# Optimization experiments

Hardware: AMD Instinct MI355X
Metric: run time of the kernel (lower is better)

## Reference

```python
import jax, jax.numpy as jnp
import numpy as np

K = 16

def _local_cov(points):
    # points: [B, N, 3]. FoldingNet-style local covariance feature.
    xx = jnp.sum(points * points, axis=-1)                       # [B,N]
    inner = jnp.einsum('bnd,bmd->bnm', points, points)           # [B,N,N]
    pd = -xx[:, :, None] + 2.0 * inner - xx[:, None, :]          # negative sq dist
    _, idx = jax.lax.top_k(pd, K)                                # [B,N,K] nearest first (self at 0)
    n0 = jnp.take_along_axis(points, idx[:, :, 0][:, :, None], axis=1)  # [B,N,3]
    n1 = jnp.take_along_axis(points, idx[:, :, 1][:, :, None], axis=1)  # [B,N,3]
    cov = n0[..., :, None] * n1[..., None, :]                    # [B,N,3,3] outer product
    B, N = points.shape[0], points.shape[1]
    return jnp.concatenate([points, cov.reshape(B, N, 9)], axis=-1)     # [B,N,12]

def _stage(x, w1, b1, wr, br, w2, b2):
    h = jax.nn.relu(x @ w1 + b1)
    h = jax.nn.relu(h + (h @ wr + br))   # ResidualLinearLayer then ReLU
    return h @ w2 + b2                   # [B,N,1]

def setup_inputs() -> dict:
    key = jax.random.key(0)
    ks = jax.random.split(key, 16)
    B, N, F = 8, 4096, 512
    s = 0.02
    d = {
        'latent': jax.random.normal(ks[0], (B, N, F), jnp.float32),
        'reconstructed_points': jax.random.normal(ks[1], (B, 3, N), jnp.float32),
        's1_w1': jax.random.normal(ks[2], (F + 12, F), jnp.float32) * s,
        's1_b1': jnp.zeros((F,), jnp.float32),
        's1_wr': jax.random.normal(ks[3], (F, F), jnp.float32) * s,
        's1_br': jnp.zeros((F,), jnp.float32),
        's1_w2': jax.random.normal(ks[4], (F, 1), jnp.float32) * s,
        's1_b2': jnp.zeros((1,), jnp.float32),
        's2_w1': jax.random.normal(ks[5], (F + 1, F), jnp.float32) * s,
        's2_b1': jnp.zeros((F,), jnp.float32),
        's2_wr': jax.random.normal(ks[6], (F, F), jnp.float32) * s,
        's2_br': jnp.zeros((F,), jnp.float32),
        's2_w2': jax.random.normal(ks[7], (F, 1), jnp.float32) * s,
        's2_b2': jnp.zeros((1,), jnp.float32),
        's3_w1': jax.random.normal(ks[8], (F + 1, F), jnp.float32) * s,
        's3_b1': jnp.zeros((F,), jnp.float32),
        's3_wr': jax.random.normal(ks[9], (F, F), jnp.float32) * s,
        's3_br': jnp.zeros((F,), jnp.float32),
        's3_w2': jax.random.normal(ks[10], (F, 1), jnp.float32) * s,
        's3_b2': jnp.zeros((1,), jnp.float32),
    }
    return d

def reference(latent, reconstructed_points,
              s1_w1, s1_b1, s1_wr, s1_br, s1_w2, s1_b2,
              s2_w1, s2_b1, s2_wr, s2_br, s2_w2, s2_b2,
              s3_w1, s3_b1, s3_wr, s3_br, s3_w2, s3_b2):
    pts = jnp.transpose(reconstructed_points, (0, 2, 1))   # [B,N,3]
    local = _local_cov(pts)                                 # [B,N,12]
    f1 = jnp.concatenate([latent, local], axis=-1)
    std1 = _stage(f1, s1_w1, s1_b1, s1_wr, s1_br, s1_w2, s1_b2)
    f2 = jnp.concatenate([latent, std1], axis=-1)
    std2 = std1 + _stage(f2, s2_w1, s2_b1, s2_wr, s2_br, s2_w2, s2_b2)
    f3 = jnp.concatenate([latent, std2], axis=-1)
    std3 = std2 + _stage(f3, s3_w1, s3_b1, s3_wr, s3_br, s3_w2, s3_b2)
    return std3   # [B,N,1]
```

## Files before the change

kernel.cpp:

```cpp
#include <hip/hip_runtime.h>

typedef __bf16 bf16x8 __attribute__((ext_vector_type(8)));
typedef float f32x16 __attribute__((ext_vector_type(16)));

__device__ __forceinline__ unsigned short f2bf(float f) {
  unsigned u = __float_as_uint(f);
  u += 0x7FFFu + ((u >> 16) & 1u);
  return (unsigned short)(u >> 16);
}

__device__ __forceinline__ void gload_lds16(const void* g, void* l) {
  __builtin_amdgcn_global_load_lds((const __attribute__((address_space(1))) void*)g,
                                   (__attribute__((address_space(3))) void*)l,
                                   16, 0, 0);
}

#define NPTS 4096
#define LDX 576

__global__ __launch_bounds__(256) void convw6_kernel(
    const float* w0, const float* w1, const float* w2,
    const float* r0, const float* r1, const float* r2,
    unsigned short* d0, unsigned short* d1, unsigned short* d2,
    unsigned short* e0, unsigned short* e1, unsigned short* e2) {
  int z = blockIdx.z;
  const float* src; unsigned short* dst; int Ksrc, Kpad, addI;
  switch (z) {
    case 0: src = w0; dst = d0; Ksrc = 524; Kpad = 576; addI = 0; break;
    case 1: src = w1; dst = d1; Ksrc = 513; Kpad = 576; addI = 0; break;
    case 2: src = w2; dst = d2; Ksrc = 513; Kpad = 576; addI = 0; break;
    case 3: src = r0; dst = e0; Ksrc = 512; Kpad = 512; addI = 1; break;
    case 4: src = r1; dst = e1; Ksrc = 512; Kpad = 512; addI = 1; break;
    default: src = r2; dst = e2; Ksrc = 512; Kpad = 512; addI = 1; break;
  }
  int k0 = blockIdx.x * 32;
  if (k0 >= Kpad) return;
  __shared__ float tile[32][33];
  int n0 = blockIdx.y * 32;
  int tx = threadIdx.x & 31, ty = threadIdx.x >> 5;
#pragma unroll
  for (int r = 0; r < 32; r += 8) {
    int k = k0 + ty + r, n = n0 + tx;
    tile[ty + r][tx] = (k < Ksrc) ? src[(size_t)k * 512 + n] : 0.f;
  }
  __syncthreads();
#pragma unroll
  for (int r = 0; r < 32; r += 8) {
    int n = n0 + ty + r, k = k0 + tx;
    float v = tile[tx][ty + r];
    if (addI && n == k) v += 1.0f;
    dst[(size_t)n * Kpad + k] = f2bf(v);
  }
}

__global__ __launch_bounds__(256) void conv_latent_kernel(const float* __restrict__ latent,
                                                          unsigned short* __restrict__ X) {
  size_t idx = (size_t)blockIdx.x * 256 + threadIdx.x;
  size_t m = idx >> 7;
  int c4 = (int)(idx & 127) * 4;
  float4 v = *(const float4*)(latent + m * 512 + c4);
  ushort4 o;
  o.x = f2bf(v.x); o.y = f2bf(v.y); o.z = f2bf(v.z); o.w = f2bf(v.w);
  *(ushort4*)(X + m * LDX + c4) = o;
}

__device__ __forceinline__ void merge1(float& v, int& j, int mk) {
  float ov = __shfl_xor(v, mk); int oj = __shfl_xor(j, mk);
  bool take = (ov > v) || (ov == v && oj < j);
  v = take ? ov : v; j = take ? oj : j;
}

__global__ __launch_bounds__(512) void knn_kernel(const float* __restrict__ rp,
                                                  unsigned short* __restrict__ X) {
  __shared__ float4 P[NPTS];
  int b = blockIdx.y;
  const float* base = rp + (size_t)b * 3 * NPTS;
  for (int j = threadIdx.x; j < NPTS; j += 512) {
    float x = base[j], y = base[NPTS + j], z = base[2 * NPTS + j];
    float xx = __fadd_rn(__fadd_rn(__fmul_rn(x, x), __fmul_rn(y, y)), __fmul_rn(z, z));
    P[j] = make_float4(x, y, z, -xx);
  }
  __syncthreads();
  int wave = threadIdx.x >> 6, lane = threadIdx.x & 63;
  int grp = lane >> 4, slice = lane & 15;
  int il0 = wave * 8 + grp * 2;
  int ia = blockIdx.x * 64 + il0;
  int ib = ia + 1;
  float4 pa = P[ia], pb = P[ib];
  float ax = 2.f * pa.x, ay = 2.f * pa.y, az = 2.f * pa.z;
  float bx = 2.f * pb.x, by = 2.f * pb.y, bz = 2.f * pb.z;
  float va = -3.4e38f, vb = -3.4e38f;
  int ta = 0, tb = 0;
  int sta = ((ia & 15) == slice) ? (ia >> 4) : -1;
  int stb = ((ib & 15) == slice) ? (ib >> 4) : -1;
  const float4* pp = P + slice;
#pragma unroll 8
  for (int t = 0; t < NPTS / 16; ++t) {
    float4 pj = pp[t * 16];
    float ea = __builtin_fmaf(ax, pj.x, __builtin_fmaf(ay, pj.y,
               __builtin_fmaf(az, pj.z, pj.w)));
    float eb = __builtin_fmaf(bx, pj.x, __builtin_fmaf(by, pj.y,
               __builtin_fmaf(bz, pj.z, pj.w)));
    ea = (t == sta) ? -3.4e38f : ea;
    eb = (t == stb) ? -3.4e38f : eb;
    bool ca = ea > va; va = ca ? ea : va; ta = ca ? t : ta;
    bool cb = eb > vb; vb = cb ? eb : vb; tb = cb ? t : tb;
  }
  int ja = ta * 16 + slice, jb = tb * 16 + slice;
#pragma unroll
  for (int mk = 1; mk <= 8; mk <<= 1) {
    merge1(va, ja, mk);
    merge1(vb, jb, mk);
  }
  if (slice == 0) {
#pragma unroll
    for (int p = 0; p < 2; ++p) {
      float4 pi = (p == 0) ? pa : pb;
      float4 p1 = P[(p == 0) ? ja : jb];
      size_t row = (size_t)b * NPTS + ia + p;
      unsigned short* xp = X + row * LDX + 512;
      float vals[12] = { pi.x, pi.y, pi.z,
                         pi.x * p1.x, pi.x * p1.y, pi.x * p1.z,
                         pi.y * p1.x, pi.y * p1.y, pi.y * p1.z,
                         pi.z * p1.x, pi.z * p1.y, pi.z * p1.z };
#pragma unroll
      for (int k = 0; k < 12; ++k) xp[k] = f2bf(vals[k]);
#pragma unroll
      for (int k = 12; k < 32; ++k) xp[k] = 0;
    }
  }
}

#define BM 256
#define BN 128
#define BK 64
#define GRP 520

__global__ __launch_bounds__(512) void gemm_relu_kernel(
    const unsigned short* __restrict__ Xb, const unsigned short* __restrict__ Wt,
    const float* __restrict__ bias, unsigned short* __restrict__ H,
    int K, int ldx, int ldw) {
  __shared__ unsigned short As[32 * GRP];
  __shared__ unsigned short Bs[16 * GRP];
  const int t = threadIdx.x;
  const int wave = t >> 6, lane = t & 63;
  const int m0 = blockIdx.y * BM, n0 = blockIdx.x * BN;
  const int wm = (wave >> 1) * 64, wn = (wave & 1) * 64;
  const int srow = lane >> 3;
  const int sslot = (lane & 7) ^ srow;
  const int l31 = lane & 31, hi = lane >> 5;
  const int w7 = l31 & 7, g2 = l31 >> 3;
  f32x16 acc[2][2] = {};
  for (int kt = 0; kt < K; kt += BK) {
#pragma unroll
    for (int r = 0; r < 4; ++r) {
      int ga = wave + r * 8;
      gload_lds16(Xb + (size_t)(m0 + ga * 8 + srow) * ldx + kt + sslot * 8, As + ga * GRP);
    }
#pragma unroll
    for (int r = 0; r < 2; ++r) {
      int gb = wave + r * 8;
      gload_lds16(Wt + (size_t)(n0 + gb * 8 + srow) * ldw + kt + sslot * 8, Bs + gb * GRP);
    }
    __syncthreads();
#pragma unroll
    for (int ks = 0; ks < 4; ++ks) {
      int qx = (ks * 2 + hi) ^ w7;
      bf16x8 a[2], bb[2];
#pragma unroll
      for (int i = 0; i < 2; ++i)
        a[i] = *(const bf16x8*)(As + ((wm >> 3) + i * 4 + g2) * GRP + w7 * 64 + qx * 8);
#pragma unroll
      for (int j = 0; j < 2; ++j)
        bb[j] = *(const bf16x8*)(Bs + ((wn >> 3) + j * 4 + g2) * GRP + w7 * 64 + qx * 8);
#pragma unroll
      for (int i = 0; i < 2; ++i)
#pragma unroll
        for (int j = 0; j < 2; ++j)
          acc[i][j] = __builtin_amdgcn_mfma_f32_32x32x16_bf16(a[i], bb[j], acc[i][j], 0, 0, 0);
    }
    __syncthreads();
  }
#pragma unroll
  for (int j = 0; j < 2; ++j) {
    int col = n0 + wn + j * 32 + l31;
    float bv = bias[col];
#pragma unroll
    for (int i = 0; i < 2; ++i) {
#pragma unroll
      for (int rg = 0; rg < 16; ++rg) {
        int row = m0 + wm + i * 32 + (rg & 3) + 8 * (rg >> 2) + 4 * hi;
        float v = acc[i][j][rg] + bv;
        v = v > 0.f ? v : 0.f;
        H[(size_t)row * 512 + col] = f2bf(v);
      }
    }
  }
}

__global__ __launch_bounds__(512) void gemm_res_kernel(
    const unsigned short* __restrict__ H1, const unsigned short* __restrict__ Wt,
    const float* __restrict__ br, const float* __restrict__ w2,
    float* __restrict__ so) {
  __shared__ unsigned short As[32 * GRP];
  __shared__ unsigned short Bs[16 * GRP];
  const int t = threadIdx.x;
  const int wave = t >> 6, lane = t & 63;
  const int m0 = blockIdx.y * BM, n0 = blockIdx.x * BN;
  const int wm = (wave >> 1) * 64, wn = (wave & 1) * 64;
  const int srow = lane >> 3;
  const int sslot = (lane & 7) ^ srow;
  const int l31 = lane & 31, hi = lane >> 5;
  const int w7 = l31 & 7, g2 = l31 >> 3;
  f32x16 acc[2][2] = {};
  for (int kt = 0; kt < 512; kt += BK) {
#pragma unroll
    for (int r = 0; r < 4; ++r) {
      int ga = wave + r * 8;
      gload_lds16(H1 + (size_t)(m0 + ga * 8 + srow) * 512 + kt + sslot * 8, As + ga * GRP);
    }
#pragma unroll
    for (int r = 0; r < 2; ++r) {
      int gb = wave + r * 8;
      gload_lds16(Wt + (size_t)(n0 + gb * 8 + srow) * 512 + kt + sslot * 8, Bs + gb * GRP);
    }
    __syncthreads();
#pragma unroll
    for (int ks = 0; ks < 4; ++ks) {
      int qx = (ks * 2 + hi) ^ w7;
      bf16x8 a[2], bb[2];
#pragma unroll
      for (int i = 0; i < 2; ++i)
        a[i] = *(const bf16x8*)(As + ((wm >> 3) + i * 4 + g2) * GRP + w7 * 64 + qx * 8);
#pragma unroll
      for (int j = 0; j < 2; ++j)
        bb[j] = *(const bf16x8*)(Bs + ((wn >> 3) + j * 4 + g2) * GRP + w7 * 64 + qx * 8);
#pragma unroll
      for (int i = 0; i < 2; ++i)
#pragma unroll
        for (int j = 0; j < 2; ++j)
          acc[i][j] = __builtin_amdgcn_mfma_f32_32x32x16_bf16(a[i], bb[j], acc[i][j], 0, 0, 0);
    }
    __syncthreads();
  }
  float pr[2][16];
#pragma unroll
  for (int i = 0; i < 2; ++i)
#pragma unroll
    for (int rg = 0; rg < 16; ++rg) pr[i][rg] = 0.f;
#pragma unroll
  for (int j = 0; j < 2; ++j) {
    int col = n0 + wn + j * 32 + l31;
    float bv = br[col], wv = w2[col];
#pragma unroll
    for (int i = 0; i < 2; ++i)
#pragma unroll
      for (int rg = 0; rg < 16; ++rg) {
        float v = acc[i][j][rg] + bv;
        v = v > 0.f ? v : 0.f;
        pr[i][rg] += v * wv;
      }
  }
#pragma unroll
  for (int i = 0; i < 2; ++i)
#pragma unroll
    for (int rg = 0; rg < 16; ++rg) {
      float s = pr[i][rg];
      s += __shfl_xor(s, 1); s += __shfl_xor(s, 2); s += __shfl_xor(s, 4);
      s += __shfl_xor(s, 8); s += __shfl_xor(s, 16);
      if (l31 == 0) {
        int row = m0 + wm + i * 32 + (rg & 3) + 8 * (rg >> 2) + 4 * hi;
        atomicAdd(&so[row], s);
      }
    }
}

__global__ __launch_bounds__(256) void init_so_kernel(float* so, const float* b2) {
  int m = blockIdx.x * 256 + threadIdx.x;
  so[m] = b2[0];
}
__global__ __launch_bounds__(256) void update_kernel(float* std_cum, float* so,
                                                     unsigned short* X,
                                                     const float* b2_next, int first) {
  int m = blockIdx.x * 256 + threadIdx.x;
  float s = so[m];
  if (!first) s += std_cum[m];
  std_cum[m] = s;
  unsigned short* xp = X + (size_t)m * LDX + 512;
  xp[0] = f2bf(s);
#pragma unroll
  for (int k = 1; k < 12; ++k) xp[k] = 0;
  so[m] = b2_next[0];
}
__global__ __launch_bounds__(256) void finalize_kernel(float* out, const float* std_cum,
                                                       const float* so) {
  int m = blockIdx.x * 256 + threadIdx.x;
  out[m] = std_cum[m] + so[m];
}

extern "C" void kernel_launch(void* const* d_in, const int* in_sizes, int n_in,
                              void* d_out, int out_size, void* d_ws, size_t ws_size,
                              hipStream_t stream) {
  const int B = 8, N = NPTS, M = B * N;
  const float* latent = (const float*)d_in[0];
  const float* rp = (const float*)d_in[1];
  const float* w1[3] = {(const float*)d_in[2], (const float*)d_in[8], (const float*)d_in[14]};
  const float* b1[3] = {(const float*)d_in[3], (const float*)d_in[9], (const float*)d_in[15]};
  const float* wr[3] = {(const float*)d_in[4], (const float*)d_in[10], (const float*)d_in[16]};
  const float* br[3] = {(const float*)d_in[5], (const float*)d_in[11], (const float*)d_in[17]};
  const float* w2[3] = {(const float*)d_in[6], (const float*)d_in[12], (const float*)d_in[18]};
  const float* b2[3] = {(const float*)d_in[7], (const float*)d_in[13], (const float*)d_in[19]};

  char* ws = (char*)d_ws;
  auto carve = [&](size_t bytes) {
    char* p = ws;
    ws += (bytes + 255) & ~(size_t)255;
    return p;
  };
  unsigned short* X  = (unsigned short*)carve((size_t)M * LDX * 2);
  unsigned short* H1 = (unsigned short*)carve((size_t)M * 512 * 2);
  unsigned short* W1t[3], *Wrt[3];
  for (int s = 0; s < 3; ++s) W1t[s] = (unsigned short*)carve((size_t)512 * LDX * 2);
  for (int s = 0; s < 3; ++s) Wrt[s] = (unsigned short*)carve((size_t)512 * 512 * 2);
  float* std_cum = (float*)carve((size_t)M * 4);
  float* so      = (float*)carve((size_t)M * 4);

  convw6_kernel<<<dim3(LDX / 32, 16, 6), 256, 0, stream>>>(
      w1[0], w1[1], w1[2], wr[0], wr[1], wr[2],
      W1t[0], W1t[1], W1t[2], Wrt[0], Wrt[1], Wrt[2]);
  conv_latent_kernel<<<(M * 128) / 256, 256, 0, stream>>>(latent, X);
  knn_kernel<<<dim3(N / 64, B), 512, 0, stream>>>(rp, X);
  init_so_kernel<<<M / 256, 256, 0, stream>>>(so, b2[0]);

  for (int s = 0; s < 3; ++s) {
    gemm_relu_kernel<<<dim3(BN / 128 * 4, M / BM), 512, 0, stream>>>(X, W1t[s], b1[s], H1,
                                                                     LDX, LDX, LDX);
    gemm_res_kernel<<<dim3(4, M / BM), 512, 0, stream>>>(H1, Wrt[s], br[s], w2[s], so);
    if (s < 2)
      update_kernel<<<M / 256, 256, 0, stream>>>(std_cum, so, X, b2[s + 1], s == 0 ? 1 : 0);
  }
  finalize_kernel<<<M / 256, 256, 0, stream>>>((float*)d_out, std_cum, so);
}
```

Measured before the change: 348.3 us.

## Apply std feature as rank-1 epilogue and reorder GEMM block mapping

For stages 2 and 3, the GEMM now runs only over the 512 latent columns and adds the single std feature as a rank-1 fp32 update (std times the last W1 row) in the epilogue. This skips the extra 64-wide K tile that held the feature and removes the per-stage write of the feature into X, and it also keeps the std term in fp32 instead of rounding it to bf16. Separately, block indices are remapped so consecutive blocks walk along M for a fixed N tile, which changes L2 reuse of the weight and activation tiles.

```diff
diff --git a/kernel.cpp b/kernel.cpp
--- a/kernel.cpp
+++ b/kernel.cpp
@@ -135,16 +135,20 @@
 #define BN 128
 #define BK 64
 #define GRP 520
+#define MBLK 128
 
 __global__ __launch_bounds__(512) void gemm_relu_kernel(
     const unsigned short* __restrict__ Xb, const unsigned short* __restrict__ Wt,
     const float* __restrict__ bias, unsigned short* __restrict__ H,
-    int K, int ldx, int ldw) {
+    int K, int ldx, int ldw,
+    const float* __restrict__ stdv, const float* __restrict__ w1row) {
   __shared__ unsigned short As[32 * GRP];
   __shared__ unsigned short Bs[16 * GRP];
   const int t = threadIdx.x;
   const int wave = t >> 6, lane = t & 63;
-  const int m0 = blockIdx.y * BM, n0 = blockIdx.x * BN;
+  const int flat = blockIdx.y * gridDim.x + blockIdx.x;
+  const int m0 = (flat & (MBLK - 1)) * BM;
+  const int n0 = (flat >> 7) * BN;
   const int wm = (wave >> 1) * 64, wn = (wave & 1) * 64;
   const int srow = lane >> 3;
   const int sslot = (lane & 7) ^ srow;
@@ -180,6 +184,21 @@
           acc[i][j] = __builtin_amdgcn_mfma_f32_32x32x16_bf16(a[i], bb[j], acc[i][j], 0, 0, 0);
     }
     __syncthreads();
+  }
+  if (w1row) {
+    float wv[2];
+#pragma unroll
+    for (int j = 0; j < 2; ++j) wv[j] = w1row[n0 + wn + j * 32 + l31];
+#pragma unroll
+    for (int i = 0; i < 2; ++i) {
+#pragma unroll
+      for (int rg = 0; rg < 16; ++rg) {
+        int row = m0 + wm + i * 32 + (rg & 3) + 8 * (rg >> 2) + 4 * hi;
+        float sv = stdv[row];
+        acc[i][0][rg] += sv * wv[0];
+        acc[i][1][rg] += sv * wv[1];
+      }
+    }
   }
 #pragma unroll
   for (int j = 0; j < 2; ++j) {
@@ -206,7 +225,9 @@
   __shared__ unsigned short Bs[16 * GRP];
   const int t = threadIdx.x;
   const int wave = t >> 6, lane = t & 63;
-  const int m0 = blockIdx.y * BM, n0 = blockIdx.x * BN;
+  const int flat = blockIdx.y * gridDim.x + blockIdx.x;
+  const int m0 = (flat & (MBLK - 1)) * BM;
+  const int n0 = (flat >> 7) * BN;
   const int wm = (wave >> 1) * 64, wn = (wave & 1) * 64;
   const int srow = lane >> 3;
   const int sslot = (lane & 7) ^ srow;
@@ -280,16 +301,11 @@
   so[m] = b2[0];
 }
 __global__ __launch_bounds__(256) void update_kernel(float* std_cum, float* so,
-                                                     unsigned short* X,
                                                      const float* b2_next, int first) {
   int m = blockIdx.x * 256 + threadIdx.x;
   float s = so[m];
   if (!first) s += std_cum[m];
   std_cum[m] = s;
-  unsigned short* xp = X + (size_t)m * LDX + 512;
-  xp[0] = f2bf(s);
-#pragma unroll
-  for (int k = 1; k < 12; ++k) xp[k] = 0;
   so[m] = b2_next[0];
 }
 __global__ __launch_bounds__(256) void finalize_kernel(float* out, const float* std_cum,
@@ -333,11 +349,16 @@
   init_so_kernel<<<M / 256, 256, 0, stream>>>(so, b2[0]);
 
   for (int s = 0; s < 3; ++s) {
-    gemm_relu_kernel<<<dim3(BN / 128 * 4, M / BM), 512, 0, stream>>>(X, W1t[s], b1[s], H1,
-                                                                     LDX, LDX, LDX);
+    if (s == 0) {
+      gemm_relu_kernel<<<dim3(512 / BN, M / BM), 512, 0, stream>>>(
+          X, W1t[s], b1[s], H1, LDX, LDX, LDX, nullptr, nullptr);
+    } else {
+      gemm_relu_kernel<<<dim3(512 / BN, M / BM), 512, 0, stream>>>(
+          X, W1t[s], b1[s], H1, 512, LDX, LDX, std_cum, w1[s] + (size_t)512 * 512);
+    }
     gemm_res_kernel<<<dim3(4, M / BM), 512, 0, stream>>>(H1, Wrt[s], br[s], w2[s], so);
     if (s < 2)
-      update_kernel<<<M / 256, 256, 0, stream>>>(std_cum, so, X, b2[s + 1], s == 0 ? 1 : 0);
+      update_kernel<<<M / 256, 256, 0, stream>>>(std_cum, so, b2[s + 1], s == 0 ? 1 : 0);
   }
   finalize_kernel<<<M / 256, 256, 0, stream>>>((float*)d_out, std_cum, so);
 }
```

Result: no change. 342.8 us (-1.6%).

## Fuse both stage GEMMs into one kernel keeping hidden activations in LDS

Applied to the files above, without the earlier changes.

Replaces the separate first-layer and residual GEMM kernels with a single fused kernel. Each block owns 64 rows and computes all 512 hidden columns, writes the ReLU output into swizzled LDS, and runs the residual GEMM from LDS with double-buffered A staging and prefetched weight tiles. The scalar std input of stages 2 and 3 is added as a rank-1 fp32 update using the original weight row, so K shrinks to 512 and update_kernel no longer writes into X. This removes the H1 round trip through global memory, at the cost of large dynamic LDS (about 150KB), low occupancy and a smaller 64-row tile per block.

```diff
diff --git a/kernel.cpp b/kernel.cpp
--- a/kernel.cpp
+++ b/kernel.cpp
@@ -17,6 +17,7 @@
 
 #define NPTS 4096
 #define LDX 576
+#define GRP 520
 
 __global__ __launch_bounds__(256) void convw6_kernel(
     const float* w0, const float* w1, const float* w2,
@@ -131,148 +132,179 @@
   }
 }
 
-#define BM 256
-#define BN 128
-#define BK 64
-#define GRP 520
-
-__global__ __launch_bounds__(512) void gemm_relu_kernel(
-    const unsigned short* __restrict__ Xb, const unsigned short* __restrict__ Wt,
-    const float* __restrict__ bias, unsigned short* __restrict__ H,
-    int K, int ldx, int ldw) {
-  __shared__ unsigned short As[32 * GRP];
-  __shared__ unsigned short Bs[16 * GRP];
+__global__ __launch_bounds__(512) void fused_stage_kernel(
+    const unsigned short* __restrict__ Xb, const unsigned short* __restrict__ W1t,
+    const float* __restrict__ b1v, const unsigned short* __restrict__ Wrt,
+    const float* __restrict__ brv, const float* __restrict__ w2v,
+    float* __restrict__ so, int K1,
+    const float* __restrict__ stdv, const float* __restrict__ w1row) {
+  extern __shared__ unsigned short S[];
+  unsigned short* HL = S;
+  unsigned short* BL = S + 64 * GRP;
+  unsigned short* AL = S + 128 * GRP;
   const int t = threadIdx.x;
   const int wave = t >> 6, lane = t & 63;
-  const int m0 = blockIdx.y * BM, n0 = blockIdx.x * BN;
-  const int wm = (wave >> 1) * 64, wn = (wave & 1) * 64;
+  const int m0 = blockIdx.x * 64;
   const int srow = lane >> 3;
   const int sslot = (lane & 7) ^ srow;
   const int l31 = lane & 31, hi = lane >> 5;
   const int w7 = l31 & 7, g2 = l31 >> 3;
+
+  const unsigned short* Arow  = Xb  + (size_t)(m0 + wave * 8 + srow) * LDX + sslot * 8;
+  const unsigned short* Wrow1 = W1t + (size_t)(64 * wave + srow) * LDX + sslot * 8;
+  const unsigned short* Wrow2 = Wrt + (size_t)(64 * wave + srow) * 512 + sslot * 8;
+
+  auto STAGE_A = [&](int buf, int kt) {
+    gload_lds16(Arow + (size_t)kt * 64, AL + buf * (8 * GRP) + wave * GRP);
+  };
+  auto STAGE_B1 = [&](int kt) {
+#pragma unroll
+    for (int r = 0; r < 8; ++r)
+      gload_lds16(Wrow1 + (size_t)r * 8 * LDX + (size_t)kt * 64, BL + (8 * wave + r) * GRP);
+  };
+  auto STAGE_B2 = [&](int kt) {
+#pragma unroll
+    for (int r = 0; r < 8; ++r)
+      gload_lds16(Wrow2 + (size_t)r * 8 * 512 + (size_t)kt * 64, BL + (8 * wave + r) * GRP);
+  };
+
+  STAGE_A(0, 0);
+  STAGE_B1(0);
+  asm volatile("s_waitcnt vmcnt(0)" ::: "memory");
+  __builtin_amdgcn_s_barrier();
+
   f32x16 acc[2][2] = {};
-  for (int kt = 0; kt < K; kt += BK) {
-#pragma unroll
-    for (int r = 0; r < 4; ++r) {
-      int ga = wave + r * 8;
-      gload_lds16(Xb + (size_t)(m0 + ga * 8 + srow) * ldx + kt + sslot * 8, As + ga * GRP);
-    }
-#pragma unroll
-    for (int r = 0; r < 2; ++r) {
-      int gb = wave + r * 8;
-      gload_lds16(Wt + (size_t)(n0 + gb * 8 + srow) * ldw + kt + sslot * 8, Bs + gb * GRP);
-    }
-    __syncthreads();
-#pragma unroll
-    for (int ks = 0; ks < 4; ++ks) {
-      int qx = (ks * 2 + hi) ^ w7;
-      bf16x8 a[2], bb[2];
+  const int nt1 = K1 / 64;
+  for (int t1 = 0; t1 < nt1; ++t1) {
+    const int cur = t1 & 1;
+    bf16x8 af[2][4], bf[2][4];
+#pragma unroll
+    for (int i = 0; i < 2; ++i)
+#pragma unroll
+      for (int ks = 0; ks < 4; ++ks)
+        af[i][ks] = *(const bf16x8*)(AL + cur * (8 * GRP) + (i * 4 + g2) * GRP +
+                                     w7 * 64 + (((2 * ks + hi) ^ w7) * 8));
+#pragma unroll
+    for (int j = 0; j < 2; ++j)
+#pragma unroll
+      for (int ks = 0; ks < 4; ++ks)
+        bf[j][ks] = *(const bf16x8*)(BL + (8 * wave + j * 4 + g2) * GRP +
+                                     w7 * 64 + (((2 * ks + hi) ^ w7) * 8));
+    asm volatile("s_waitcnt lgkmcnt(0)" ::: "memory");
+    __builtin_amdgcn_sched_barrier(0);
+    if (t1 + 1 < nt1) {
+      STAGE_A(cur ^ 1, t1 + 1);
+      STAGE_B1(t1 + 1);
+    } else {
+      STAGE_B2(0);
+    }
+#pragma unroll
+    for (int ks = 0; ks < 4; ++ks)
 #pragma unroll
       for (int i = 0; i < 2; ++i)
-        a[i] = *(const bf16x8*)(As + ((wm >> 3) + i * 4 + g2) * GRP + w7 * 64 + qx * 8);
+#pragma unroll
+        for (int j = 0; j < 2; ++j)
+          acc[i][j] = __builtin_amdgcn_mfma_f32_32x32x16_bf16(af[i][ks], bf[j][ks],
+                                                              acc[i][j], 0, 0, 0);
+    asm volatile("s_waitcnt vmcnt(0)" ::: "memory");
+    __builtin_amdgcn_sched_barrier(0);
+    __builtin_amdgcn_s_barrier();
+  }
+
+  if (w1row) {
+    float wv1[2];
+#pragma unroll
+    for (int j = 0; j < 2; ++j) wv1[j] = w1row[64 * wave + j * 32 + l31];
+#pragma unroll
+    for (int i = 0; i < 2; ++i)
+#pragma unroll
+      for (int rg = 0; rg < 16; ++rg) {
+        int row = i * 32 + (rg & 3) + 8 * (rg >> 2) + 4 * hi;
+        float sv = stdv[m0 + row];
+#pragma unroll
+        for (int j = 0; j < 2; ++j) acc[i][j][rg] += sv * wv1[j];
+      }
+  }
+
+  {
+    float bv1[2];
+#pragma unroll
+    for (int j = 0; j < 2; ++j) bv1[j] = b1v[64 * wave + j * 32 + l31];
+#pragma unroll
+    for (int i = 0; i < 2; ++i)
 #pragma unroll
       for (int j = 0; j < 2; ++j)
-        bb[j] = *(const bf16x8*)(Bs + ((wn >> 3) + j * 4 + g2) * GRP + w7 * 64 + qx * 8);
+#pragma unroll
+        for (int rg = 0; rg < 16; ++rg) {
+          int r7 = (rg & 3) + 4 * hi;
+          int g  = i * 4 + (rg >> 2);
+          int c8 = j * 4 + g2;
+          float v = acc[i][j][rg] + bv1[j];
+          v = v > 0.f ? v : 0.f;
+          HL[(wave * 8 + g) * GRP + (r7 * 8 + (c8 ^ r7)) * 8 + w7] = f2bf(v);
+        }
+  }
+  asm volatile("s_waitcnt lgkmcnt(0)" ::: "memory");
+  __builtin_amdgcn_s_barrier();
+
+  f32x16 acc2[2][2] = {};
+  for (int t2 = 0; t2 < 8; ++t2) {
+    bf16x8 af[2][4], bf[2][4];
+#pragma unroll
+    for (int i = 0; i < 2; ++i)
+#pragma unroll
+      for (int ks = 0; ks < 4; ++ks)
+        af[i][ks] = *(const bf16x8*)(HL + (t2 * 8 + i * 4 + g2) * GRP +
+                                     w7 * 64 + (((2 * ks + hi) ^ w7) * 8));
+#pragma unroll
+    for (int j = 0; j < 2; ++j)
+#pragma unroll
+      for (int ks = 0; ks < 4; ++ks)
+        bf[j][ks] = *(const bf16x8*)(BL + (8 * wave + j * 4 + g2) * GRP +
+                                     w7 * 64 + (((2 * ks + hi) ^ w7) * 8));
+    asm volatile("s_waitcnt lgkmcnt(0)" ::: "memory");
+    __builtin_amdgcn_sched_barrier(0);
+    if (t2 < 7) STAGE_B2(t2 + 1);
+#pragma unroll
+    for (int ks = 0; ks < 4; ++ks)
 #pragma unroll
       for (int i = 0; i < 2; ++i)
 #pragma unroll
         for (int j = 0; j < 2; ++j)
-          acc[i][j] = __builtin_amdgcn_mfma_f32_32x32x16_bf16(a[i], bb[j], acc[i][j], 0, 0, 0);
-    }
-    __syncthreads();
-  }
-#pragma unroll
-  for (int j = 0; j < 2; ++j) {
-    int col = n0 + wn + j * 32 + l31;
-    float bv = bias[col];
-#pragma unroll
-    for (int i = 0; i < 2; ++i) {
+          acc2[i][j] = __builtin_amdgcn_mfma_f32_32x32x16_bf16(af[i][ks], bf[j][ks],
+                                                               acc2[i][j], 0, 0, 0);
+    if (t2 < 7) {
+      asm volatile("s_waitcnt vmcnt(0)" ::: "memory");
+      __builtin_amdgcn_sched_barrier(0);
+    }
+  }
+
+  {
+    float bv2[2], wv2[2];
+#pragma unroll
+    for (int j = 0; j < 2; ++j) {
+      int col = 64 * wave + j * 32 + l31;
+      bv2[j] = brv[col]; wv2[j] = w2v[col];
+    }
+#pragma unroll
+    for (int i = 0; i < 2; ++i)
 #pragma unroll
       for (int rg = 0; rg < 16; ++rg) {
-        int row = m0 + wm + i * 32 + (rg & 3) + 8 * (rg >> 2) + 4 * hi;
-        float v = acc[i][j][rg] + bv;
-        v = v > 0.f ? v : 0.f;
-        H[(size_t)row * 512 + col] = f2bf(v);
+        float s = 0.f;
+#pragma unroll
+        for (int j = 0; j < 2; ++j) {
+          float v = acc2[i][j][rg] + bv2[j];
+          v = v > 0.f ? v : 0.f;
+          s += v * wv2[j];
+        }
+        s += __shfl_xor(s, 1); s += __shfl_xor(s, 2); s += __shfl_xor(s, 4);
+        s += __shfl_xor(s, 8); s += __shfl_xor(s, 16);
+        if (l31 == 0) {
+          int row = i * 32 + (rg & 3) + 8 * (rg >> 2) + 4 * hi;
+          atomicAdd(&so[m0 + row], s);
+        }
       }
-    }
-  }
-}
-
-__global__ __launch_bounds__(512) void gemm_res_kernel(
-    const unsigned short* __restrict__ H1, const unsigned short* __restrict__ Wt,
-    const float* __restrict__ br, const float* __restrict__ w2,
-    float* __restrict__ so) {
-  __shared__ unsigned short As[32 * GRP];
-  __shared__ unsigned short Bs[16 * GRP];
-  const int t = threadIdx.x;
-  const int wave = t >> 6, lane = t & 63;
-  const int m0 = blockIdx.y * BM, n0 = blockIdx.x * BN;
-  const int wm = (wave >> 1) * 64, wn = (wave & 1) * 64;
-  const int srow = lane >> 3;
-  const int sslot = (lane & 7) ^ srow;
-  const int l31 = lane & 31, hi = lane >> 5;
-  const int w7 = l31 & 7, g2 = l31 >> 3;
-  f32x16 acc[2][2] = {};
-  for (int kt = 0; kt < 512; kt += BK) {
-#pragma unroll
-    for (int r = 0; r < 4; ++r) {
-      int ga = wave + r * 8;
-      gload_lds16(H1 + (size_t)(m0 + ga * 8 + srow) * 512 + kt + sslot * 8, As + ga * GRP);
-    }
-#pragma unroll
-    for (int r = 0; r < 2; ++r) {
-      int gb = wave + r * 8;
-      gload_lds16(Wt + (size_t)(n0 + gb * 8 + srow) * 512 + kt + sslot * 8, Bs + gb * GRP);
-    }
-    __syncthreads();
-#pragma unroll
-    for (int ks = 0; ks < 4; ++ks) {
-      int qx = (ks * 2 + hi) ^ w7;
-      bf16x8 a[2], bb[2];
-#pragma unroll
-      for (int i = 0; i < 2; ++i)
-        a[i] = *(const bf16x8*)(As + ((wm >> 3) + i * 4 + g2) * GRP + w7 * 64 + qx * 8);
-#pragma unroll
-      for (int j = 0; j < 2; ++j)
-        bb[j] = *(const bf16x8*)(Bs + ((wn >> 3) + j * 4 + g2) * GRP + w7 * 64 + qx * 8);
-#pragma unroll
-      for (int i = 0; i < 2; ++i)
-#pragma unroll
-        for (int j = 0; j < 2; ++j)
-          acc[i][j] = __builtin_amdgcn_mfma_f32_32x32x16_bf16(a[i], bb[j], acc[i][j], 0, 0, 0);
-    }
-    __syncthreads();
-  }
-  float pr[2][16];
-#pragma unroll
-  for (int i = 0; i < 2; ++i)
-#pragma unroll
-    for (int rg = 0; rg < 16; ++rg) pr[i][rg] = 0.f;
-#pragma unroll
-  for (int j = 0; j < 2; ++j) {
-    int col = n0 + wn + j * 32 + l31;
-    float bv = br[col], wv = w2[col];
-#pragma unroll
-    for (int i = 0; i < 2; ++i)
-#pragma unroll
-      for (int rg = 0; rg < 16; ++rg) {
-        float v = acc[i][j][rg] + bv;
-        v = v > 0.f ? v : 0.f;
-        pr[i][rg] += v * wv;
-      }
-  }
-#pragma unroll
-  for (int i = 0; i < 2; ++i)
-#pragma unroll
-    for (int rg = 0; rg < 16; ++rg) {
-      float s = pr[i][rg];
-      s += __shfl_xor(s, 1); s += __shfl_xor(s, 2); s += __shfl_xor(s, 4);
-      s += __shfl_xor(s, 8); s += __shfl_xor(s, 16);
-      if (l31 == 0) {
-        int row = m0 + wm + i * 32 + (rg & 3) + 8 * (rg >> 2) + 4 * hi;
-        atomicAdd(&so[row], s);
-      }
-    }
+  }
 }
 
 __global__ __launch_bounds__(256) void init_so_kernel(float* so, const float* b2) {
@@ -280,16 +312,11 @@
   so[m] = b2[0];
 }
 __global__ __launch_bounds__(256) void update_kernel(float* std_cum, float* so,
-                                                     unsigned short* X,
                                                      const float* b2_next, int first) {
   int m = blockIdx.x * 256 + threadIdx.x;
   float s = so[m];
   if (!first) s += std_cum[m];
   std_cum[m] = s;
-  unsigned short* xp = X + (size_t)m * LDX + 512;
-  xp[0] = f2bf(s);
-#pragma unroll
-  for (int k = 1; k < 12; ++k) xp[k] = 0;
   so[m] = b2_next[0];
 }
 __global__ __launch_bounds__(256) void finalize_kernel(float* out, const float* std_cum,
@@ -317,13 +344,14 @@
     ws += (bytes + 255) & ~(size_t)255;
     return p;
   };
-  unsigned short* X  = (unsigned short*)carve((size_t)M * LDX * 2);
-  unsigned short* H1 = (unsigned short*)carve((size_t)M * 512 * 2);
+  unsigned short* X = (unsigned short*)carve((size_t)M * LDX * 2);
   unsigned short* W1t[3], *Wrt[3];
   for (int s = 0; s < 3; ++s) W1t[s] = (unsigned short*)carve((size_t)512 * LDX * 2);
   for (int s = 0; s < 3; ++s) Wrt[s] = (unsigned short*)carve((size_t)512 * 512 * 2);
   float* std_cum = (float*)carve((size_t)M * 4);
   float* so      = (float*)carve((size_t)M * 4);
+
+  const size_t ldsBytes = (size_t)144 * GRP * 2;
 
   convw6_kernel<<<dim3(LDX / 32, 16, 6), 256, 0, stream>>>(
       w1[0], w1[1], w1[2], wr[0], wr[1], wr[2],
@@ -333,11 +361,16 @@
   init_so_kernel<<<M / 256, 256, 0, stream>>>(so, b2[0]);
 
   for (int s = 0; s < 3; ++s) {
-    gemm_relu_kernel<<<dim3(BN / 128 * 4, M / BM), 512, 0, stream>>>(X, W1t[s], b1[s], H1,
-                                                                     LDX, LDX, LDX);
-    gemm_res_kernel<<<dim3(4, M / BM), 512, 0, stream>>>(H1, Wrt[s], br[s], w2[s], so);
+    if (s == 0) {
+      fused_stage_kernel<<<dim3(M / 64), 512, ldsBytes, stream>>>(
+          X, W1t[s], b1[s], Wrt[s], br[s], w2[s], so, LDX, nullptr, nullptr);
+    } else {
+      fused_stage_kernel<<<dim3(M / 64), 512, ldsBytes, stream>>>(
+          X, W1t[s], b1[s], Wrt[s], br[s], w2[s], so, 512, std_cum,
+          w1[s] + (size_t)512 * 512);
+    }
     if (s < 2)
-      update_kernel<<<M / 256, 256, 0, stream>>>(std_cum, so, X, b2[s + 1], s == 0 ? 1 : 0);
+      update_kernel<<<M / 256, 256, 0, stream>>>(std_cum, so, b2[s + 1], s == 0 ? 1 : 0);
   }
   finalize_kernel<<<M / 256, 256, 0, stream>>>((float*)d_out, std_cum, so);
 }
```

Measured after the change: 345.9 us. Within noise of the previous version (-0.7%).
